# Optimization experiments

Hardware: AMD Instinct MI355X
Metric: run time of the kernel (lower is better)

## Reference

```python
import jax, jax.numpy as jnp
import numpy as np


def setup_inputs() -> dict:
    key = jax.random.key(0)
    k1, k2 = jax.random.split(key)
    B, N = 2048, 2048
    y_prime = jax.random.normal(k1, (B, N, 3), dtype=jnp.float32)
    y = jax.random.normal(k2, (B, N, 3), dtype=jnp.float32)
    return {"y_prime": y_prime, "y": y}


def reference(y_prime, y):
    """Batched SVD-superimposer (Kabsch) RMSD, averaged over the batch.

    Faithful to Biopython's SVDSuperimposer as used by RMSDLoss:
      set(reference=y, coords=y_prime); run(); get_rms().
    """
    n_atoms = y.shape[1]
    # Center both point clouds (av1/av2 in SVDSuperimposer)
    c = y_prime - jnp.mean(y_prime, axis=1, keepdims=True)  # coords, [B,N,3]
    r = y - jnp.mean(y, axis=1, keepdims=True)              # reference, [B,N,3]
    # a = coords^T @ reference  -> [B,3,3]
    a = jnp.einsum('bni,bnj->bij', c, r)
    u, s, vt = jnp.linalg.svd(a, full_matrices=False)
    # rot = (vt^T u^T)^T = u @ vt; fix improper rotation (reflection) via det sign
    det = jnp.linalg.det(jnp.einsum('bik,bkj->bij', u, vt))  # [B]
    sign = jnp.sign(det)
    ones = jnp.ones_like(sign)
    flip = jnp.stack([ones, ones, sign], axis=-1)            # [B,3]
    rot = jnp.einsum('bik,bk,bkj->bij', u, flip, vt)         # [B,3,3]
    # transformed = centered_coords @ rot; compare to centered reference
    diff = jnp.einsum('bni,bij->bnj', c, rot) - r
    rms = jnp.sqrt(jnp.sum(diff * diff, axis=(1, 2)) / n_atoms)  # [B]
    return jnp.mean(rms)
```

## Files before the change

kernel.cpp:

```cpp
#include <hip/hip_runtime.h>
#include <cmath>


constexpr int BLOCK = 256;
constexpr int NWAVE = BLOCK / 64;
constexpr int NS = 17;

template<int N>
__global__ __launch_bounds__(BLOCK, 8) void rmsd_kernel(
    const float* __restrict__ yp,
    const float* __restrict__ yr,
    float* __restrict__ rms_out)
{
    static_assert(N == BLOCK * 8, "one thread = 8 atoms = 6 float4");
    const int b   = blockIdx.x;
    const int tid = threadIdx.x;
    const size_t row = (size_t)b * (size_t)N * 3u;
    const float4* p4 = (const float4*)(yp + row) + tid * 6;
    const float4* q4 = (const float4*)(yr + row) + tid * 6;

    float s1x=0.f,s1y=0.f,s1z=0.f, s2x=0.f,s2y=0.f,s2z=0.f, sq1=0.f,sq2=0.f;
    float c00=0.f,c01=0.f,c02=0.f,c10=0.f,c11=0.f,c12=0.f,c20=0.f,c21=0.f,c22=0.f;

    auto accum4 = [&](const float4&a0,const float4&a1,const float4&a2,
                      const float4&b0,const float4&b1,const float4&b2){
        float px[4]={a0.x,a0.w,a1.z,a2.y};
        float py[4]={a0.y,a1.x,a1.w,a2.z};
        float pz[4]={a0.z,a1.y,a2.x,a2.w};
        float qx[4]={b0.x,b0.w,b1.z,b2.y};
        float qy[4]={b0.y,b1.x,b1.w,b2.z};
        float qz[4]={b0.z,b1.y,b2.x,b2.w};
        #pragma unroll
        for (int k=0;k<4;k++){
            s1x+=px[k]; s1y+=py[k]; s1z+=pz[k];
            s2x+=qx[k]; s2y+=qy[k]; s2z+=qz[k];
            sq1 = fmaf(px[k],px[k], fmaf(py[k],py[k], fmaf(pz[k],pz[k], sq1)));
            sq2 = fmaf(qx[k],qx[k], fmaf(qy[k],qy[k], fmaf(qz[k],qz[k], sq2)));
            c00=fmaf(px[k],qx[k],c00); c01=fmaf(px[k],qy[k],c01); c02=fmaf(px[k],qz[k],c02);
            c10=fmaf(py[k],qx[k],c10); c11=fmaf(py[k],qy[k],c11); c12=fmaf(py[k],qz[k],c12);
            c20=fmaf(pz[k],qx[k],c20); c21=fmaf(pz[k],qy[k],c21); c22=fmaf(pz[k],qz[k],c22);
        }
    };

    {
        const float4 P0=p4[0], P1=p4[1], P2=p4[2];
        const float4 Q0=q4[0], Q1=q4[1], Q2=q4[2];
        __builtin_amdgcn_sched_barrier(0);
        accum4(P0,P1,P2, Q0,Q1,Q2);
    }
    {
        const float4 P3=p4[3], P4=p4[4], P5=p4[5];
        const float4 Q3=q4[3], Q4=q4[4], Q5=q4[5];
        __builtin_amdgcn_sched_barrier(0);
        accum4(P3,P4,P5, Q3,Q4,Q5);
    }

    float vals[NS] = {s1x,s1y,s1z,s2x,s2y,s2z,sq1,sq2,
                      c00,c01,c02,c10,c11,c12,c20,c21,c22};
    __shared__ float sred[NWAVE][NS];
    const int wave = tid >> 6, lane = tid & 63;
    #pragma unroll
    for (int i = 0; i < NS; ++i) {
        float v = vals[i];
        #pragma unroll
        for (int off = 32; off > 0; off >>= 1) v += __shfl_down(v, off, 64);
        if (lane == 0) sred[wave][i] = v;
    }
    __syncthreads();

    if (tid == 0) {
        float t[NS];
        #pragma unroll
        for (int i = 0; i < NS; ++i) {
            float s = 0.f;
            #pragma unroll
            for (int w = 0; w < NWAVE; ++w) s += sred[w][i];
            t[i] = s;
        }
        const float fn = (float)N;
        const float m1x=t[0]/fn, m1y=t[1]/fn, m1z=t[2]/fn;
        const float m2x=t[3]/fn, m2y=t[4]/fn, m2z=t[5]/fn;
        const float E0 = (t[6] - fn*(m1x*m1x+m1y*m1y+m1z*m1z))
                       + (t[7] - fn*(m2x*m2x+m2y*m2y+m2z*m2z));
        const float A00=t[8] -fn*m1x*m2x, A01=t[9] -fn*m1x*m2y, A02=t[10]-fn*m1x*m2z;
        const float A10=t[11]-fn*m1y*m2x, A11=t[12]-fn*m1y*m2y, A12=t[13]-fn*m1y*m2z;
        const float A20=t[14]-fn*m1z*m2x, A21=t[15]-fn*m1z*m2y, A22=t[16]-fn*m1z*m2z;

        const float det = A00*(A11*A22-A12*A21)
                        - A01*(A10*A22-A12*A20)
                        + A02*(A10*A21-A11*A20);

        const float G00 = A00*A00+A10*A10+A20*A20;
        const float G01 = A00*A01+A10*A11+A20*A21;
        const float G02 = A00*A02+A10*A12+A20*A22;
        const float G11 = A01*A01+A11*A11+A21*A21;
        const float G12 = A01*A02+A11*A12+A21*A22;
        const float G22 = A02*A02+A12*A12+A22*A22;

        const float q  = (G00+G11+G22)*(1.f/3.f);
        const float p1 = G01*G01 + G02*G02 + G12*G12;
        const float p2 = (G00-q)*(G00-q)+(G11-q)*(G11-q)+(G22-q)*(G22-q) + 2.f*p1;
        const float p  = sqrtf(p2*(1.f/6.f));
        float e1, e2, e3;
        if (p < 1e-20f) {
            e1 = e2 = e3 = q;
        } else {
            const float ip = 1.f/p;
            const float C00=(G00-q)*ip, C01=G01*ip, C02=G02*ip;
            const float C11=(G11-q)*ip, C12=G12*ip, C22=(G22-q)*ip;
            float detC = C00*(C11*C22-C12*C12)
                       - C01*(C01*C22-C12*C02)
                       + C02*(C01*C12-C11*C02);
            float rr = fminf(1.f, fmaxf(-1.f, 0.5f*detC));
            const float phi = acosf(rr)*(1.f/3.f);
            e1 = q + 2.f*p*cosf(phi);
            e3 = q + 2.f*p*cosf(phi + 2.0943951023931953f);
            e2 = 3.f*q - e1 - e3;
        }
        const float sv0 = sqrtf(fmaxf(e1,0.f));
        const float sv1 = sqrtf(fmaxf(e2,0.f));
        const float sv2 = sqrtf(fmaxf(e3,0.f));
        const float trs = sv0 + sv1 + ((det >= 0.f) ? sv2 : -sv2);
        const float msd = fmaxf(0.f, (E0 - 2.f*trs)/fn);
        rms_out[b] = sqrtf(msd);
    }
}

__global__ __launch_bounds__(BLOCK) void mean_kernel(
    const float* __restrict__ rms, float* __restrict__ out, int B)
{
    const int tid = threadIdx.x;
    const float4* r4 = (const float4*)rms;
    float s = 0.f;
    for (int i = tid; i < B/4; i += BLOCK) {
        float4 v = r4[i];
        s += (v.x + v.y) + (v.z + v.w);
    }
    #pragma unroll
    for (int off = 32; off > 0; off >>= 1) s += __shfl_down(s, off, 64);
    __shared__ float sred[NWAVE];
    const int wave = tid >> 6, lane = tid & 63;
    if (lane == 0) sred[wave] = s;
    __syncthreads();
    if (tid == 0) {
        float tot = 0.f;
        #pragma unroll
        for (int w = 0; w < NWAVE; ++w) tot += sred[w];
        out[0] = tot / (float)B;
    }
}

extern "C" void kernel_launch(void* const* d_in, const int* in_sizes, int n_in,
                              void* d_out, int out_size, void* d_ws, size_t ws_size,
                              hipStream_t stream) {
    const float* yp = (const float*)d_in[0];
    const float* yr = (const float*)d_in[1];
    const int N = 2048;
    const int B = in_sizes[0] / (N * 3);
    float* rms_ws = (float*)d_ws;

    rmsd_kernel<2048><<<B, BLOCK, 0, stream>>>(yp, yr, rms_ws);
    mean_kernel<<<1, BLOCK, 0, stream>>>(rms_ws, (float*)d_out, B);
}
```

Measured before the change: 26.81 us.

## Fuse batch mean into RMSD kernel via last-block atomic counters

Drops the separate mean kernel launch. Each block publishes its RMS value and bumps a two-level atomic counter, and the last block to finish sums all per-batch RMS values and writes the mean. This removes a kernel launch and its dependency gap, but adds a memset node plus atomics and fences to every block.

```diff
diff --git a/kernel.cpp b/kernel.cpp
--- a/kernel.cpp
+++ b/kernel.cpp
@@ -10,7 +10,11 @@
 __global__ __launch_bounds__(BLOCK, 8) void rmsd_kernel(
     const float* __restrict__ yp,
     const float* __restrict__ yr,
-    float* __restrict__ rms_out)
+    float* __restrict__ rms,
+    int*   __restrict__ cnt1,
+    int*   __restrict__ cnt2,
+    float* __restrict__ out,
+    int Btot, float invB)
 {
     static_assert(N == BLOCK * 8, "one thread = 8 atoms = 6 float4");
     const int b   = blockIdx.x;
@@ -68,6 +72,7 @@
     }
     __syncthreads();
 
+    __shared__ int sflag;
     if (tid == 0) {
         float t[NS];
         #pragma unroll
@@ -122,31 +127,38 @@
         const float sv2 = sqrtf(fmaxf(e3,0.f));
         const float trs = sv0 + sv1 + ((det >= 0.f) ? sv2 : -sv2);
         const float msd = fmaxf(0.f, (E0 - 2.f*trs)/fn);
-        rms_out[b] = sqrtf(msd);
+        __hip_atomic_store(&rms[b], sqrtf(msd),
+                           __ATOMIC_RELAXED, __HIP_MEMORY_SCOPE_AGENT);
+        __threadfence();
+
+        const int g   = b >> 6;
+        const int bsz = min(64, Btot - (g << 6));
+        int flag = 0;
+        if (atomicAdd(&cnt1[g * 32], 1) == bsz - 1) {
+            const int nbuckets = (Btot + 63) >> 6;
+            if (atomicAdd(cnt2, 1) == nbuckets - 1) flag = 1;
+        }
+        sflag = flag;
     }
-}
+    __syncthreads();
 
-__global__ __launch_bounds__(BLOCK) void mean_kernel(
-    const float* __restrict__ rms, float* __restrict__ out, int B)
-{
-    const int tid = threadIdx.x;
-    const float4* r4 = (const float4*)rms;
-    float s = 0.f;
-    for (int i = tid; i < B/4; i += BLOCK) {
-        float4 v = r4[i];
-        s += (v.x + v.y) + (v.z + v.w);
-    }
-    #pragma unroll
-    for (int off = 32; off > 0; off >>= 1) s += __shfl_down(s, off, 64);
-    __shared__ float sred[NWAVE];
-    const int wave = tid >> 6, lane = tid & 63;
-    if (lane == 0) sred[wave] = s;
-    __syncthreads();
-    if (tid == 0) {
-        float tot = 0.f;
+    if (sflag) {
+        __threadfence();
+        float acc = 0.f;
+        for (int i = tid; i < Btot; i += BLOCK)
+            acc += __hip_atomic_load(&rms[i],
+                                     __ATOMIC_RELAXED, __HIP_MEMORY_SCOPE_AGENT);
         #pragma unroll
-        for (int w = 0; w < NWAVE; ++w) tot += sred[w];
-        out[0] = tot / (float)B;
+        for (int off = 32; off > 0; off >>= 1) acc += __shfl_down(acc, off, 64);
+        __shared__ float sred2[NWAVE];
+        if (lane == 0) sred2[wave] = acc;
+        __syncthreads();
+        if (tid == 0) {
+            float tot = 0.f;
+            #pragma unroll
+            for (int w = 0; w < NWAVE; ++w) tot += sred2[w];
+            out[0] = tot * invB;
+        }
     }
 }
 
@@ -157,8 +169,12 @@
     const float* yr = (const float*)d_in[1];
     const int N = 2048;
     const int B = in_sizes[0] / (N * 3);
-    float* rms_ws = (float*)d_ws;
 
-    rmsd_kernel<2048><<<B, BLOCK, 0, stream>>>(yp, yr, rms_ws);
-    mean_kernel<<<1, BLOCK, 0, stream>>>(rms_ws, (float*)d_out, B);
+    int*   cnt1 = (int*)d_ws;
+    int*   cnt2 = (int*)((char*)d_ws + 4096);
+    float* rms  = (float*)((char*)d_ws + 8192);
+
+    hipMemsetAsync(d_ws, 0, 4352, stream);
+    rmsd_kernel<2048><<<B, BLOCK, 0, stream>>>(
+        yp, yr, rms, cnt1, cnt2, (float*)d_out, B, 1.0f/(float)B);
 }
```

New measurement: 72.89 us. 2.72x slower.
